# Kernel optimization log

Hardware: AMD Instinct MI355X
Metric: run time of the kernel (lower is better)

Reference implementation:

```python
import jax, jax.numpy as jnp
import numpy as np

BITWIDTH = 8
T = 1 << BITWIDTH          # bit-stream length = 2**bitwidth = 256
B = 16                     # independent unary streams
IN1, H1, H2, OUT = 1024, 512, 256, 10


def sobol_rng(bitwidth=BITWIDTH):
    # 1-D unscrambled Sobol sequence (== torch.quasirandom.SobolEngine(1)),
    n = 1 << bitwidth
    i = np.arange(n, dtype=np.uint32)
    g = i ^ (i >> 1)  # Gray code
    x = np.zeros(n, dtype=np.float64)
    for j in range(bitwidth):
        x += ((g >> np.uint32(j)) & np.uint32(1)).astype(np.float64) * 2.0 ** -(j + 1)
    return jnp.asarray(x * 2.0 - 1.0, dtype=jnp.float32)


def _forward(w1, b1, w2, b2, w3, b3, prediction, x):
    rng = sobol_rng()
    f32 = jnp.float32
    Bn = x.shape[1]

    def lin_state(fin, fout):
        # rng_wght_idx rows are all identical in the torch code (the [1, fin]
        # input broadcasts across [fout, fin]), so we keep only [B, fin].
        return (jnp.zeros((Bn, fin), jnp.int32),   # rng_wght_idx
                jnp.zeros((Bn, fin), jnp.int32),   # rng_wght_idx_inv
                jnp.zeros((Bn, fout), f32),        # in_accumulator
                jnp.zeros((Bn, fout), f32))        # out_accumulator

    def ulinear(state, xf, xi, w, bvec, t, offset):
        cum, cum_inv, in_acc, out_acc = state
        # regenerate binary weight matrices by compare against gathered rng
        w_pos = (w[None, :, :] > rng[cum][:, None, :]).astype(f32)      # [B, fout, fin]
        w_neg = (w[None, :, :] <= rng[cum_inv][:, None, :]).astype(f32)  # [B, fout, fin]
        bias_bit = (bvec > rng[t]).astype(f32)                           # [fout]
        y = (jnp.einsum('bi,boi->bo', xf, w_pos)
             + jnp.einsum('bi,boi->bo', 1.0 - xf, w_neg)
             + bias_bit[None, :])
        in_acc = in_acc + y - offset
        out = (in_acc > out_acc).astype(f32)
        out_acc = out_acc + out
        return (cum + xi, cum_inv + (1 - xi), in_acc, out_acc), out

    def ucompare(acc, inp):  # unary ReLU (UnaryCompare)
        sign = (acc < 0).astype(f32)
        out = sign + (1.0 - sign) * inp
        return acc + 2.0 * out - 1.0, out

    def step(carry, xs_t):
        s1, c1, s2, c2, s3 = carry
        xi, t = xs_t
        xf = xi.astype(f32)
        s1, y1 = ulinear(s1, xf, xi, w1, b1, t, (IN1 - 1) / 2)
        c1, a1 = ucompare(c1, y1)
        s2, y2 = ulinear(s2, a1, a1.astype(jnp.int32), w2, b2, t, (H1 - 1) / 2)
        c2, a2 = ucompare(c2, y2)
        s3, y3 = ulinear(s3, a2, a2.astype(jnp.int32), w3, b3, t, (H2 - 1) / 2)
        # ProgressivePrecision is re-created every forward: out_pp = 2*y3 - 1,
        # err = out_pp - prediction, then log_softmax.
        out_t = jax.nn.log_softmax(2.0 * y3 - 1.0 - prediction, axis=1)
        return (s1, c1, s2, c2, s3), out_t

    init = (lin_state(IN1, H1), jnp.zeros((Bn, H1), f32),
            lin_state(H1, H2), jnp.zeros((Bn, H2), f32),
            lin_state(H2, OUT))
    _, outs = jax.lax.scan(step, init, (x, jnp.arange(T)))
    return outs  # [T, B, OUT]


def setup_inputs():
    key = jax.random.key(0)
    ks = jax.random.split(key, 8)
    u = lambda k, s: jax.random.uniform(k, s, jnp.float32, -1.0, 1.0)
    return {
        'w1': u(ks[0], (H1, IN1)), 'b1': u(ks[1], (H1,)),
        'w2': u(ks[2], (H2, H1)), 'b2': u(ks[3], (H2,)),
        'w3': u(ks[4], (OUT, H2)), 'b3': u(ks[5], (OUT,)),
        'prediction': 0.1 * jax.random.normal(ks[6], (B, OUT), jnp.float32),
        'x': jax.random.randint(ks[7], (T, B, IN1), 0, 2, jnp.int32),
    }


def reference(w1, b1, w2, b2, w3, b3, prediction, x):
    return _forward(w1, b1, w2, b2, w3, b3, prediction, x)
```

## Files before the change

kernel.cpp:

```cpp
#include <hip/hip_runtime.h>
#include <stdint.h>

#define TSTEPS 256
#define NB 16
#define NM (TSTEPS*NB)

typedef short s16x2 __attribute__((ext_vector_type(2)));

__device__ __forceinline__ uint32_t perm8(int i) {
  uint32_t g = (uint32_t)(i ^ (i >> 1));
  return __brev(g) >> 24;
}

__device__ __forceinline__ void qmad(uint32_t& z, uint32_t a, uint32_t t_s,
                                     uint32_t e) {
  asm("v_pk_mad_i16 %0, %1, %2, %3" : "=v"(z) : "v"(a), "s"(t_s), "v"(e));
}
__device__ __forceinline__ uint32_t qperm(uint32_t x, uint32_t y, uint32_t sel) {
  uint32_t d;
  asm("v_perm_b32 %0, %1, %2, %3" : "=v"(d) : "v"(x), "v"(y), "v"(sel));
  return d;
}
__device__ __forceinline__ void qsad(uint32_t& acc, uint32_t p) {
  asm("v_sad_u8 %0, %1, 0, %0" : "+v"(acc) : "v"(p));
}

__device__ __forceinline__ void qstep3(uint32_t& acc, uint32_t t2, uint32_t a2,
                                       uint32_t e2, uint32_t c15) {
  uint32_t z;
  asm("v_pk_mad_i16 %0, %2, %3, %4\n\t"
      "v_pk_ashrrev_i16 %0, %5, %0\n\t"
      "v_pk_add_i16 %1, %1, %0"
      : "=&v"(z), "+v"(acc)
      : "v"(a2), "v"(t2), "v"(e2), "v"(c15));
}

__device__ __forceinline__ uint32_t pkadd16(uint32_t a, uint32_t b) {
  return __builtin_bit_cast(uint32_t,
        (s16x2)(__builtin_bit_cast(s16x2, a) + __builtin_bit_cast(s16x2, b)));
}

__device__ __forceinline__ void unpackAE(uint32_t v2, uint32_t& a2, uint32_t& e2) {
  s16x2 sv = __builtin_bit_cast(s16x2, v2) >> 15;
  uint32_t su = __builtin_bit_cast(uint32_t, sv);
  uint32_t vand = v2 & 0x01FF01FFu;
  e2 = pkadd16(~vand, su & 0x01FF01FFu);
  a2 = pkadd16(0x00010001u, pkadd16(su, su));
}

__device__ __forceinline__ int rank256(float w) {
  double v = 128.0 * (double)w + 128.0;
  int t = (int)ceil(v);
  if (t < 0) t = 0; if (t > 256) t = 256;
  return t;
}

#define SUMLOHI(A,B,C,D, LO, HI) \
  LO = (A & 0xFFFFu) + (B & 0xFFFFu) + (C & 0xFFFFu) + (D & 0xFFFFu); \
  HI = (A >> 16) + (B >> 16) + (C >> 16) + (D >> 16);

__global__ __launch_bounds__(256) void k_prepA(
    const float* __restrict__ w1, const float* __restrict__ w2,
    const float* __restrict__ w3, const float* __restrict__ b1,
    const float* __restrict__ b2, const float* __restrict__ b3,
    const int* __restrict__ x,
    uint32_t* __restrict__ T1, uint32_t* __restrict__ T2,
    uint32_t* __restrict__ T3t, uint32_t* __restrict__ bb1,
    uint32_t* __restrict__ bb2, uint32_t* __restrict__ bb3,
    uint16_t* __restrict__ cs)
{
  int bid = blockIdx.x, tid = threadIdx.x;
  if (bid < 1024) {
    int e = bid * 256 + tid;
    T1[e] = (uint32_t)rank256(w1[2 * e]) |
            ((uint32_t)rank256(w1[2 * e + 1]) << 16);
  } else if (bid < 1280) {
    int e = (bid - 1024) * 256 + tid;
    T2[e] = (uint32_t)rank256(w2[2 * e]) |
            ((uint32_t)rank256(w2[2 * e + 1]) << 16);
  } else if (bid < 1285) {
    int e = (bid - 1280) * 256 + tid;
    if (e < 1280) {
      int n = e % 10, kp = e / 10;
      T3t[e] = (uint32_t)rank256(w3[n * 256 + 2 * kp]) |
               ((uint32_t)rank256(w3[n * 256 + 2 * kp + 1]) << 16);
    }
  } else if (bid < 1301) {
    int w = (bid - 1285) * 256 + tid;
    int o = w >> 3, j = w & 7;
    double bv = (double)b1[o] * 128.0 + 128.0;
    uint32_t bits = 0;
    for (int s = 0; s < 32; ++s)
      if (bv > (double)perm8(j * 32 + s)) bits |= 1u << s;
    bb1[w] = bits;
  } else if (bid < 1309) {
    int w = (bid - 1301) * 256 + tid;
    int o = w >> 3, j = w & 7;
    double bv = (double)b2[o] * 128.0 + 128.0;
    uint32_t bits = 0;
    for (int s = 0; s < 32; ++s)
      if (bv > (double)perm8(j * 32 + s)) bits |= 1u << s;
    bb2[w] = bits;
  } else if (bid == 1309) {
    if (tid < 80) {
      int o = tid >> 3, j = tid & 7;
      double bv = (double)b3[o] * 128.0 + 128.0;
      uint32_t bits = 0;
      for (int s = 0; s < 32; ++s)
        if (bv > (double)perm8(j * 32 + s)) bits |= 1u << s;
      bb3[tid] = bits;
    }
  } else {
    int g = (bid - 1310) * 256 + tid;
    int i = g & 1023, b = (g >> 10) & 15, c = g >> 14;
    int s = 0, t0 = c * 32;
    for (int tt = t0; tt < t0 + 32; ++tt)
      s += x[((size_t)tt * NB + b) * 1024 + i];
    cs[(c * NB + b) * 1024 + i] = (uint16_t)s;
  }
}

__global__ __launch_bounds__(256) void k_prep1ae(const int* __restrict__ x,
                                                 const uint16_t* __restrict__ cs,
                                                 uint2* __restrict__ AE1) {
  int g = blockIdx.x * 256 + threadIdx.x;
  int ip = g & 511;
  int b = (g >> 9) & 15, c = g >> 13;
  int i0 = 2 * ip;
  int cum0 = 0, cum1 = 0;
  for (int cc = 0; cc < c; ++cc) {
    uint32_t two = *(const uint32_t*)(cs + (cc * NB + b) * 1024 + i0);
    cum0 += (int)(two & 0xFFFFu);
    cum1 += (int)(two >> 16);
  }
  int t0 = c * 32;
  for (int tt = t0; tt < t0 + 32; ++tt) {
    int m = b * 256 + tt;
    int2 xv = *(const int2*)(x + ((size_t)tt * NB + b) * 1024 + i0);
    int idx0 = xv.x ? cum0 : (tt - cum0);
    int idx1 = xv.y ? cum1 : (tt - cum1);
    uint32_t p0 = perm8(idx0), p1 = perm8(idx1);
    uint32_t v0 = (xv.x ? p0 : (510u - p0)) | ((uint32_t)(xv.x ^ 1) << 15);
    uint32_t v1 = (xv.y ? p1 : (510u - p1)) | ((uint32_t)(xv.y ^ 1) << 15);
    uint32_t a2, e2;
    unpackAE(v0 | (v1 << 16), a2, e2);
    AE1[(size_t)m * 512 + ip] = make_uint2(a2, e2);
    cum0 += xv.x; cum1 += xv.y;
  }
}

template<int KD, int NT, int NREG, int KC>
__global__ __launch_bounds__(256, 4) void k_gemmv6(
    const uint2* __restrict__ AE, const uint32_t* __restrict__ T,
    uint16_t* __restrict__ Yp)
{
  const int tid = threadIdx.x;
  const int m = blockIdx.x * 256 + tid;
  const int n0 = blockIdx.y * NREG;
  const int sk = blockIdx.z;
  const int k0 = sk * KC;
  uint32_t sel = 0x07050301u;
  uint32_t acc[NREG];
  #pragma unroll
  for (int nn = 0; nn < NREG; ++nn) acc[nn] = 0;
  const uint4* vsrc = (const uint4*)(AE + (size_t)m * (KD / 2) + (k0 >> 1));
  const uint32_t* tbase = T + (size_t)n0 * (KD / 2) + (k0 >> 1);
  #pragma unroll 1
  for (int c = 0; c < KC / 8; ++c) {
    uint4 w01 = vsrc[2 * c];
    uint4 w23 = vsrc[2 * c + 1];
    uint32_t a0 = w01.x, e0 = w01.y, a1 = w01.z, e1 = w01.w;
    uint32_t a2v = w23.x, e2v = w23.y, a3 = w23.z, e3 = w23.w;
    asm volatile("" : "+v"(a0), "+v"(e0), "+v"(a1), "+v"(e1),
                      "+v"(a2v), "+v"(e2v), "+v"(a3), "+v"(e3));
    #pragma unroll
    for (int nn = 0; nn < NREG; ++nn) {
      uint4 tw = *(const uint4*)(tbase + (size_t)nn * (KD / 2) + c * 4);
      uint32_t z0, z1, z2, z3;
      qmad(z0, a0, tw.x, e0);
      qmad(z1, a1, tw.y, e1);
      qmad(z2, a2v, tw.z, e2v);
      qmad(z3, a3, tw.w, e3);
      qsad(acc[nn], qperm(z0, z1, sel));
      qsad(acc[nn], qperm(z2, z3, sel));
    }
  }
  uint16_t* outp = Yp + ((size_t)sk * NT + n0) * (size_t)NM + m;
  #pragma unroll
  for (int nn = 0; nn < NREG; ++nn)
    outp[(size_t)nn * NM] = (uint16_t)acc[nn];
}

template<int KD, int NT, int NREG, int KC>
__global__ __launch_bounds__(256, 4) void k_gemmv5(
    const uint16_t* __restrict__ V, const uint32_t* __restrict__ T,
    uint16_t* __restrict__ Yp)
{
  const int tid = threadIdx.x;
  const int m = blockIdx.x * 256 + tid;
  const int n0 = blockIdx.y * NREG;
  const int sk = blockIdx.z;
  const int k0 = sk * KC;
  uint32_t sel = 0x07050301u;
  uint32_t acc[NREG];
  #pragma unroll
  for (int nn = 0; nn < NREG; ++nn) acc[nn] = 0;
  const uint4* vsrc = (const uint4*)(V + (size_t)m * KD + k0);
  const uint32_t* tbase = T + (size_t)n0 * (KD / 2) + (k0 >> 1);
  #pragma unroll 1
  for (int c = 0; c < KC / 8; ++c) {
    uint4 vv = vsrc[c];
    uint32_t a0, e0, a1, e1, a2v, e2v, a3, e3;
    unpackAE(vv.x, a0, e0);
    unpackAE(vv.y, a1, e1);
    unpackAE(vv.z, a2v, e2v);
    unpackAE(vv.w, a3, e3);
    asm volatile("" : "+v"(a0), "+v"(e0), "+v"(a1), "+v"(e1),
                      "+v"(a2v), "+v"(e2v), "+v"(a3), "+v"(e3));
    #pragma unroll
    for (int nn = 0; nn < NREG; ++nn) {
      uint4 tw = *(const uint4*)(tbase + (size_t)nn * (KD / 2) + c * 4);
      uint32_t z0, z1, z2, z3;
      qmad(z0, a0, tw.x, e0);
      qmad(z1, a1, tw.y, e1);
      qmad(z2, a2v, tw.z, e2v);
      qmad(z3, a3, tw.w, e3);
      qsad(acc[nn], qperm(z0, z1, sel));
      qsad(acc[nn], qperm(z2, z3, sel));
    }
  }
  uint16_t* outp = Yp + ((size_t)sk * NT + n0) * (size_t)NM + m;
  #pragma unroll
  for (int nn = 0; nn < NREG; ++nn)
    outp[(size_t)nn * NM] = (uint16_t)acc[nn];
}

template<int NOUT, int KD, int OFF2, int LOGN>
__global__ __launch_bounds__(64) void k_scanv3(
    const uint16_t* __restrict__ Yp, const uint32_t* __restrict__ bb,
    uint16_t* __restrict__ Vn)
{
  const size_t PS = (size_t)NOUT * NM;
  int g = blockIdx.x * 64 + threadIdx.x;
  int o = g & (NOUT - 1);
  int b = g >> LOGN;
  const uint16_t* row = Yp + (size_t)o * NM + b * 256;
  const int C = 255 * (2 * KD - OFF2);
  int inA = 0, outA = 0, cA = 0, cum = 0;
  uint4 c0 = *(const uint4*)(row);
  uint4 c1 = *(const uint4*)(row + PS);
  uint4 c2 = *(const uint4*)(row + 2 * PS);
  uint4 c3 = *(const uint4*)(row + 3 * PS);
  #pragma unroll
  for (int w = 0; w < 8; ++w) {
    uint32_t bwc = bb[o * 8 + w];
    #pragma unroll
    for (int cchunk = 0; cchunk < 4; ++cchunk) {
      int t0 = w * 32 + cchunk * 8;
      uint4 n0v = c0, n1v = c1, n2v = c2, n3v = c3;
      if (t0 < 248) {
        n0v = *(const uint4*)(row + t0 + 8);
        n1v = *(const uint4*)(row + PS + t0 + 8);
        n2v = *(const uint4*)(row + 2 * PS + t0 + 8);
        n3v = *(const uint4*)(row + 3 * PS + t0 + 8);
      }
      uint32_t s[8];
      SUMLOHI(c0.x, c1.x, c2.x, c3.x, s[0], s[1]);
      SUMLOHI(c0.y, c1.y, c2.y, c3.y, s[2], s[3]);
      SUMLOHI(c0.z, c1.z, c2.z, c3.z, s[4], s[5]);
      SUMLOHI(c0.w, c1.w, c2.w, c3.w, s[6], s[7]);
      #pragma unroll
      for (int j = 0; j < 8; ++j) {
        int t = t0 + j;
        int bit = (int)((bwc >> (t & 31)) & 1u);
        inA += C + 510 * bit - 2 * (int)s[j];
        int outb = (inA > outA) ? 1 : 0;
        outA += 510 * outb;
        int a = (cA < 0) ? 1 : outb;
        cA += 1020 * a - 510;
        int idx = a ? cum : (t - cum);
        cum += a;
        uint32_t p = perm8(idx);
        Vn[(size_t)(b * 256 + t) * NOUT + o] =
            (uint16_t)((a ? p : (510u - p)) | ((uint32_t)(a ^ 1) << 15));
      }
      c0 = n0v; c1 = n1v; c2 = n2v; c3 = n3v;
    }
  }
}

__global__ __launch_bounds__(256) void k_l3(
    const uint16_t* __restrict__ V3, const uint32_t* __restrict__ T3t,
    uint16_t* __restrict__ y3)
{
  __shared__ uint32_t T3s[128][16];
  __shared__ uint32_t UFs3[16][258];
  int tid = threadIdx.x;
  int m0 = blockIdx.x * 16;
  const uint32_t c15 = 0x000F000Fu;
  for (int j = tid; j < 2048; j += 256) {
    int kp = j >> 4, o2 = j & 15;
    T3s[kp][o2] = (o2 < 10) ? T3t[kp * 10 + o2] : 0u;
  }
  { int row = tid >> 4, part = tid & 15;
    const uint4* src = (const uint4*)(V3 + (size_t)(m0 + row) * 256 + part * 16);
    uint4 pa = src[0], pb = src[1];
    uint32_t w[8] = {pa.x, pa.y, pa.z, pa.w, pb.x, pb.y, pb.z, pb.w};
    uint32_t o[16];
    #pragma unroll
    for (int q = 0; q < 8; ++q) unpackAE(w[q], o[q * 2], o[q * 2 + 1]);
    #pragma unroll
    for (int q4 = 0; q4 < 4; ++q4)
      *(uint4*)&UFs3[row][part * 16 + q4 * 4] =
          make_uint4(o[q4 * 4], o[q4 * 4 + 1], o[q4 * 4 + 2], o[q4 * 4 + 3]);
  }
  __syncthreads();
  int mr = tid >> 4, o = tid & 15;
  uint32_t acc = 0;
  #pragma unroll 4
  for (int kp2 = 0; kp2 < 64; ++kp2) {
    uint4 uf = *(const uint4*)&UFs3[mr][kp2 * 4];
    qstep3(acc, T3s[2 * kp2][o],     uf.x, uf.y, c15);
    qstep3(acc, T3s[2 * kp2 + 1][o], uf.z, uf.w, c15);
  }
  if (o < 10)
    y3[(size_t)(m0 + mr) * 16 + o] =
        (uint16_t)(256 + (short)(acc & 0xFFFFu) + (short)(acc >> 16));
}

__global__ __launch_bounds__(256) void k_scan3sm(
    const uint16_t* __restrict__ y3, const uint32_t* __restrict__ bb3,
    const float* __restrict__ pred, float* __restrict__ out)
{
  __shared__ uint32_t obl[16][16][8];
  __shared__ float prs[160];
  int tid = threadIdx.x;
  if (tid < 160) prs[tid] = pred[tid];
  int b = tid >> 4, o = tid & 15;
  if (o < 10) {
    const uint16_t* row = y3 + (size_t)b * 256 * 16 + o;
    int in2 = 0, out2 = 0;
    #pragma unroll
    for (int w = 0; w < 8; ++w) {
      uint32_t bwc = bb3[o * 8 + w];
      uint32_t bits = 0;
      for (int s = 0; s < 32; ++s) {
        int cnt = row[(w * 32 + s) * 16];
        in2 += 2 * cnt + 2 * (int)((bwc >> s) & 1u) - 255;
        int outb = (in2 > out2) ? 1 : 0;
        out2 += outb << 1;
        bits |= (uint32_t)outb << s;
      }
      obl[b][o][w] = bits;
    }
  }
  __syncthreads();
  for (int r = tid; r < 4096; r += 256) {
    int t = r >> 4, b2 = r & 15;
    float z[10], mx = -3e38f;
    #pragma unroll
    for (int oo = 0; oo < 10; ++oo) {
      int bit = (obl[b2][oo][t >> 5] >> (t & 31)) & 1;
      z[oo] = (bit ? 1.f : -1.f) - prs[b2 * 10 + oo];
      mx = fmaxf(mx, z[oo]);
    }
    float s = 0.f;
    #pragma unroll
    for (int oo = 0; oo < 10; ++oo) s += expf(z[oo] - mx);
    float ls = logf(s);
    float* op = out + (size_t)r * 10;
    #pragma unroll
    for (int oo = 0; oo < 10; ++oo) op[oo] = z[oo] - mx - ls;
  }
}

extern "C" void kernel_launch(void* const* d_in, const int* in_sizes, int n_in,
                              void* d_out, int out_size, void* d_ws, size_t ws_size,
                              hipStream_t stream) {
  (void)in_sizes; (void)n_in; (void)out_size; (void)ws_size;
  const float* w1   = (const float*)d_in[0];
  const float* b1   = (const float*)d_in[1];
  const float* w2   = (const float*)d_in[2];
  const float* b2   = (const float*)d_in[3];
  const float* w3   = (const float*)d_in[4];
  const float* b3   = (const float*)d_in[5];
  const float* pred = (const float*)d_in[6];
  const int*   x    = (const int*)d_in[7];
  float* out = (float*)d_out;
  uint8_t* W = (uint8_t*)d_ws;

  uint32_t* T1   = (uint32_t*)(W + 0);
  uint32_t* T2   = (uint32_t*)(W + 1048576);
  uint32_t* T3t  = (uint32_t*)(W + 1310720);
  uint32_t* bb1  = (uint32_t*)(W + 1318912);
  uint32_t* bb2  = (uint32_t*)(W + 1335296);
  uint32_t* bb3  = (uint32_t*)(W + 1343488);
  uint16_t* chks = (uint16_t*)(W + 1344000);
  uint2*    AE1  = (uint2*)   (W + 1606144);
  uint16_t* Yp1  = (uint16_t*)(W + 18383360);
  uint16_t* V2   = (uint16_t*)(W + 1606144);
  uint16_t* V3   = (uint16_t*)(W + 5800448);
  uint16_t* Y3   = (uint16_t*)(W + 7897600);
  uint16_t* Yp2  = Yp1;

  hipLaunchKernelGGL(k_prepA, dim3(1822), dim3(256), 0, stream,
                     w1, w2, w3, b1, b2, b3, x, T1, T2, T3t, bb1, bb2, bb3, chks);
  hipLaunchKernelGGL(k_prep1ae, dim3(256), dim3(256), 0, stream, x, chks, AE1);
  hipLaunchKernelGGL((k_gemmv6<1024, 512, 16, 256>), dim3(16, 32, 4), dim3(256),
                     0, stream, AE1, T1, Yp1);
  hipLaunchKernelGGL((k_scanv3<512, 1024, 1023, 9>), dim3(128), dim3(64), 0,
                     stream, Yp1, bb1, V2);
  hipLaunchKernelGGL((k_gemmv5<512, 256, 16, 128>), dim3(16, 16, 4), dim3(256),
                     0, stream, V2, T2, Yp2);
  hipLaunchKernelGGL((k_scanv3<256, 512, 511, 8>), dim3(64), dim3(64), 0,
                     stream, Yp2, bb2, V3);
  hipLaunchKernelGGL(k_l3, dim3(256), dim3(256), 0, stream, V3, T3t, Y3);
  hipLaunchKernelGGL(k_scan3sm, dim3(1), dim3(256), 0, stream, Y3, bb3, pred, out);
}
```

Baseline: 198.7 us.

## Store pre-expanded A/E planes from scans, transpose y3, vectorize final scan loads

New measurement: 247.9 us. 1.25x slower.

```diff
diff --git a/kernel.cpp b/kernel.cpp
--- a/kernel.cpp
+++ b/kernel.cpp
@@ -165,7 +165,7 @@
   for (int nn = 0; nn < NREG; ++nn) acc[nn] = 0;
   const uint4* vsrc = (const uint4*)(AE + (size_t)m * (KD / 2) + (k0 >> 1));
   const uint32_t* tbase = T + (size_t)n0 * (KD / 2) + (k0 >> 1);
-  #pragma unroll 1
+  #pragma unroll 2
   for (int c = 0; c < KC / 8; ++c) {
     uint4 w01 = vsrc[2 * c];
     uint4 w23 = vsrc[2 * c + 1];
@@ -192,9 +192,9 @@
 }
 
 template<int KD, int NT, int NREG, int KC>
-__global__ __launch_bounds__(256, 4) void k_gemmv5(
-    const uint16_t* __restrict__ V, const uint32_t* __restrict__ T,
-    uint16_t* __restrict__ Yp)
+__global__ __launch_bounds__(256, 4) void k_gemmv6b(
+    const uint16_t* __restrict__ A, const uint16_t* __restrict__ E,
+    const uint32_t* __restrict__ T, uint16_t* __restrict__ Yp)
 {
   const int tid = threadIdx.x;
   const int m = blockIdx.x * 256 + tid;
@@ -205,16 +205,15 @@
   uint32_t acc[NREG];
   #pragma unroll
   for (int nn = 0; nn < NREG; ++nn) acc[nn] = 0;
-  const uint4* vsrc = (const uint4*)(V + (size_t)m * KD + k0);
+  const uint4* asrc = (const uint4*)(A + (size_t)m * KD + k0);
+  const uint4* esrc = (const uint4*)(E + (size_t)m * KD + k0);
   const uint32_t* tbase = T + (size_t)n0 * (KD / 2) + (k0 >> 1);
-  #pragma unroll 1
+  #pragma unroll 2
   for (int c = 0; c < KC / 8; ++c) {
-    uint4 vv = vsrc[c];
-    uint32_t a0, e0, a1, e1, a2v, e2v, a3, e3;
-    unpackAE(vv.x, a0, e0);
-    unpackAE(vv.y, a1, e1);
-    unpackAE(vv.z, a2v, e2v);
-    unpackAE(vv.w, a3, e3);
+    uint4 aw = asrc[c];
+    uint4 ew = esrc[c];
+    uint32_t a0 = aw.x, a1 = aw.y, a2v = aw.z, a3 = aw.w;
+    uint32_t e0 = ew.x, e1 = ew.y, e2v = ew.z, e3 = ew.w;
     asm volatile("" : "+v"(a0), "+v"(e0), "+v"(a1), "+v"(e1),
                       "+v"(a2v), "+v"(e2v), "+v"(a3), "+v"(e3));
     #pragma unroll
@@ -236,9 +235,9 @@
 }
 
 template<int NOUT, int KD, int OFF2, int LOGN>
-__global__ __launch_bounds__(64) void k_scanv3(
+__global__ __launch_bounds__(64) void k_scanv4(
     const uint16_t* __restrict__ Yp, const uint32_t* __restrict__ bb,
-    uint16_t* __restrict__ Vn)
+    uint16_t* __restrict__ Aout, uint16_t* __restrict__ Eout)
 {
   const size_t PS = (size_t)NOUT * NM;
   int g = blockIdx.x * 64 + threadIdx.x;
@@ -281,8 +280,9 @@
         int idx = a ? cum : (t - cum);
         cum += a;
         uint32_t p = perm8(idx);
-        Vn[(size_t)(b * 256 + t) * NOUT + o] =
-            (uint16_t)((a ? p : (510u - p)) | ((uint32_t)(a ^ 1) << 15));
+        size_t off = (size_t)(b * 256 + t) * NOUT + o;
+        Aout[off] = a ? (uint16_t)1 : (uint16_t)0xFFFF;
+        Eout[off] = a ? (uint16_t)(~p) : (uint16_t)p;
       }
       c0 = n0v; c1 = n1v; c2 = n2v; c3 = n3v;
     }
@@ -290,8 +290,8 @@
 }
 
 __global__ __launch_bounds__(256) void k_l3(
-    const uint16_t* __restrict__ V3, const uint32_t* __restrict__ T3t,
-    uint16_t* __restrict__ y3)
+    const uint16_t* __restrict__ A3, const uint16_t* __restrict__ E3,
+    const uint32_t* __restrict__ T3t, uint16_t* __restrict__ y3t)
 {
   __shared__ uint32_t T3s[128][16];
   __shared__ uint32_t UFs3[16][258];
@@ -303,12 +303,12 @@
     T3s[kp][o2] = (o2 < 10) ? T3t[kp * 10 + o2] : 0u;
   }
   { int row = tid >> 4, part = tid & 15;
-    const uint4* src = (const uint4*)(V3 + (size_t)(m0 + row) * 256 + part * 16);
-    uint4 pa = src[0], pb = src[1];
-    uint32_t w[8] = {pa.x, pa.y, pa.z, pa.w, pb.x, pb.y, pb.z, pb.w};
-    uint32_t o[16];
-    #pragma unroll
-    for (int q = 0; q < 8; ++q) unpackAE(w[q], o[q * 2], o[q * 2 + 1]);
+    const uint4* as = (const uint4*)(A3 + (size_t)(m0 + row) * 256 + part * 16);
+    const uint4* es = (const uint4*)(E3 + (size_t)(m0 + row) * 256 + part * 16);
+    uint4 aA = as[0], aB = as[1];
+    uint4 eA = es[0], eB = es[1];
+    uint32_t o[16] = {aA.x, eA.x, aA.y, eA.y, aA.z, eA.z, aA.w, eA.w,
+                      aB.x, eB.x, aB.y, eB.y, aB.z, eB.z, aB.w, eB.w};
     #pragma unroll
     for (int q4 = 0; q4 < 4; ++q4)
       *(uint4*)&UFs3[row][part * 16 + q4 * 4] =
@@ -323,13 +323,16 @@
     qstep3(acc, T3s[2 * kp2][o],     uf.x, uf.y, c15);
     qstep3(acc, T3s[2 * kp2 + 1][o], uf.z, uf.w, c15);
   }
-  if (o < 10)
-    y3[(size_t)(m0 + mr) * 16 + o] =
+  if (o < 10) {
+    int mm = m0 + mr;
+    int b = mm >> 8, t = mm & 255;
+    y3t[(size_t)(b * 16 + o) * 256 + t] =
         (uint16_t)(256 + (short)(acc & 0xFFFFu) + (short)(acc >> 16));
+  }
 }
 
 __global__ __launch_bounds__(256) void k_scan3sm(
-    const uint16_t* __restrict__ y3, const uint32_t* __restrict__ bb3,
+    const uint16_t* __restrict__ y3t, const uint32_t* __restrict__ bb3,
     const float* __restrict__ pred, float* __restrict__ out)
 {
   __shared__ uint32_t obl[16][16][8];
@@ -338,18 +341,29 @@
   if (tid < 160) prs[tid] = pred[tid];
   int b = tid >> 4, o = tid & 15;
   if (o < 10) {
-    const uint16_t* row = y3 + (size_t)b * 256 * 16 + o;
+    const uint16_t* row = y3t + (size_t)(b * 16 + o) * 256;
     int in2 = 0, out2 = 0;
+    uint4 cur = *(const uint4*)row;
     #pragma unroll
     for (int w = 0; w < 8; ++w) {
       uint32_t bwc = bb3[o * 8 + w];
       uint32_t bits = 0;
-      for (int s = 0; s < 32; ++s) {
-        int cnt = row[(w * 32 + s) * 16];
-        in2 += 2 * cnt + 2 * (int)((bwc >> s) & 1u) - 255;
-        int outb = (in2 > out2) ? 1 : 0;
-        out2 += outb << 1;
-        bits |= (uint32_t)outb << s;
+      #pragma unroll
+      for (int cchunk = 0; cchunk < 4; ++cchunk) {
+        int t0 = w * 32 + cchunk * 8;
+        uint4 nxt = cur;
+        if (t0 < 248) nxt = *(const uint4*)(row + t0 + 8);
+        uint32_t cw[4] = {cur.x, cur.y, cur.z, cur.w};
+        #pragma unroll
+        for (int j = 0; j < 8; ++j) {
+          int t = t0 + j;
+          int cnt = (int)((cw[j >> 1] >> ((j & 1) * 16)) & 0xFFFFu);
+          in2 += 2 * cnt + 2 * (int)((bwc >> (t & 31)) & 1u) - 255;
+          int outb = (in2 > out2) ? 1 : 0;
+          out2 += outb << 1;
+          bits |= (uint32_t)outb << (t & 31);
+        }
+        cur = nxt;
       }
       obl[b][o][w] = bits;
     }
@@ -398,9 +412,11 @@
   uint16_t* chks = (uint16_t*)(W + 1344000);
   uint2*    AE1  = (uint2*)   (W + 1606144);
   uint16_t* Yp1  = (uint16_t*)(W + 18383360);
-  uint16_t* V2   = (uint16_t*)(W + 1606144);
-  uint16_t* V3   = (uint16_t*)(W + 5800448);
-  uint16_t* Y3   = (uint16_t*)(W + 7897600);
+  uint16_t* A2   = (uint16_t*)(W + 1606144);
+  uint16_t* E2   = (uint16_t*)(W + 5800448);
+  uint16_t* A3   = (uint16_t*)(W + 9994752);
+  uint16_t* E3   = (uint16_t*)(W + 12091904);
+  uint16_t* y3t  = (uint16_t*)(W + 14189056);
   uint16_t* Yp2  = Yp1;
 
   hipLaunchKernelGGL(k_prepA, dim3(1822), dim3(256), 0, stream,
@@ -408,12 +424,12 @@
   hipLaunchKernelGGL(k_prep1ae, dim3(256), dim3(256), 0, stream, x, chks, AE1);
   hipLaunchKernelGGL((k_gemmv6<1024, 512, 16, 256>), dim3(16, 32, 4), dim3(256),
                      0, stream, AE1, T1, Yp1);
-  hipLaunchKernelGGL((k_scanv3<512, 1024, 1023, 9>), dim3(128), dim3(64), 0,
-                     stream, Yp1, bb1, V2);
-  hipLaunchKernelGGL((k_gemmv5<512, 256, 16, 128>), dim3(16, 16, 4), dim3(256),
-                     0, stream, V2, T2, Yp2);
-  hipLaunchKernelGGL((k_scanv3<256, 512, 511, 8>), dim3(64), dim3(64), 0,
-                     stream, Yp2, bb2, V3);
-  hipLaunchKernelGGL(k_l3, dim3(256), dim3(256), 0, stream, V3, T3t, Y3);
-  hipLaunchKernelGGL(k_scan3sm, dim3(1), dim3(256), 0, stream, Y3, bb3, pred, out);
-}
+  hipLaunchKernelGGL((k_scanv4<512, 1024, 1023, 9>), dim3(128), dim3(64), 0,
+                     stream, Yp1, bb1, A2, E2);
+  hipLaunchKernelGGL((k_gemmv6b<512, 256, 16, 128>), dim3(16, 16, 4), dim3(256),
+                     0, stream, A2, E2, T2, Yp2);
+  hipLaunchKernelGGL((k_scanv4<256, 512, 511, 8>), dim3(64), dim3(64), 0,
+                     stream, Yp2, bb2, A3, E3);
+  hipLaunchKernelGGL(k_l3, dim3(256), dim3(256), 0, stream, A3, E3, T3t, y3t);
+  hipLaunchKernelGGL(k_scan3sm, dim3(1), dim3(256), 0, stream, y3t, bb3, pred, out);
+}
```
